# Performance work log

Hardware: AMD Instinct MI355X
Metric: run time of the kernel (lower is better)

## Reference

```python
import jax, jax.numpy as jnp
import numpy as np

B, LV, D = 8, 4096, 256   # batch, temporal length, channels
N = 2048                   # total ROIs across the batch
P = 32                     # output_size (number of output bins)
G = int(np.ceil(LV / P))   # static max adaptive sampling grid (sampling_ratio=-1)


def setup_inputs() -> dict:
    key = jax.random.key(0)
    k1, k2, k3 = jax.random.split(key, 3)
    feat = jax.random.normal(k1, (B, LV, D), dtype=jnp.float32)
    # boxes: (start, end) along the lv axis, sorted so start <= end, in [0, LV)
    boxes = jnp.sort(
        jax.random.uniform(k2, (N, 2), dtype=jnp.float32, minval=0.0, maxval=float(LV)),
        axis=1,
    )
    batch_idx = jax.random.randint(k3, (N,), 0, B, dtype=jnp.int32)
    return {"feat": feat, "boxes": boxes, "batch_idx": batch_idx}


def _roi_align_1d(feat, boxes, batch_idx):
    # Faithful 1D specialization of torchvision roi_align with boxes
    # (0, y1, 1, y2), output_size=(P, 1), aligned=True, spatial_scale=1,
    # sampling_ratio=-1. The width axis contributes a single sample at x=0
    # with weight 1, so only the y (lv) axis math remains.
    feat_flat = feat.reshape(B * LV, D)
    y1, y2 = boxes[:, 0], boxes[:, 1]
    roi_h = y2 - y1                       # aligned=True: no max(., 1) clamp
    start = y1 - 0.5                      # aligned offset
    bin_h = roi_h / P                     # [N]
    grid_h = jnp.ceil(bin_h).astype(jnp.int32)          # adaptive samples per bin
    count = jnp.maximum(grid_h, 1).astype(feat.dtype)   # avg denominator
    sub = bin_h / jnp.maximum(grid_h, 1)                # spacing inside a bin [N]
    # bin start positions: [N, P]
    bin_off = start[:, None] + jnp.arange(P, dtype=feat.dtype)[None, :] * bin_h[:, None]
    base = batch_idx.astype(jnp.int32) * LV             # [N] row offset into feat_flat

    def bilinear(y):  # y: [N, P] -> [N, P, D]
        valid = (y >= -1.0) & (y <= float(LV))
        yc = jnp.maximum(y, 0.0)
        y_lo = jnp.floor(yc).astype(jnp.int32)
        hi_case = y_lo >= LV - 1
        y_lo = jnp.where(hi_case, LV - 1, y_lo)
        y_hi = jnp.where(hi_case, LV - 1, y_lo + 1)
        yc = jnp.where(hi_case, y_lo.astype(y.dtype), yc)
        ly = yc - y_lo.astype(y.dtype)
        v = (1.0 - ly)[..., None] * feat_flat[base[:, None] + y_lo] \
            + ly[..., None] * feat_flat[base[:, None] + y_hi]
        return jnp.where(valid[..., None], v, 0.0)

    def step(acc, g):
        y = bin_off + (g.astype(feat.dtype) + 0.5) * sub[:, None]   # [N, P]
        m = (g < grid_h)[:, None, None]                              # sample active?
        return acc + jnp.where(m, bilinear(y), 0.0), None

    acc0 = jnp.zeros((N, P, D), dtype=feat.dtype)
    acc, _ = jax.lax.scan(step, acc0, jnp.arange(G, dtype=jnp.int32))
    return acc / count[:, None, None]   # [N, P, D] (torch output after transpose(1,2))


def reference(feat, boxes, batch_idx):
    return _roi_align_1d(feat, boxes, batch_idx)
```

## Files before the change

### kernel.cpp

```cpp
#include <hip/hip_runtime.h>

#define B_  8
#define LV_ 4096
#define D_  256
#define N_  2048
#define P_  32

typedef float v4f __attribute__((ext_vector_type(4)));

__device__ __forceinline__ float lane_bcast_f(float v, int l) {
    return __int_as_float(__builtin_amdgcn_readlane(__float_as_int(v), l));
}

__global__ __launch_bounds__(256) void build_order_kernel(
    const int* __restrict__ batch_idx, int* __restrict__ order)
{
    __shared__ int cnt[B_], cur[B_];
    const int tid = threadIdx.x;
    if (tid < B_) cnt[tid] = 0;
    __syncthreads();
    for (int n = tid; n < N_; n += 256) atomicAdd(&cnt[batch_idx[n]], 1);
    __syncthreads();
    if (tid == 0) {
        int s = 0;
        for (int b = 0; b < B_; ++b) { cur[b] = s; s += cnt[b]; }
    }
    __syncthreads();
    for (int n = tid; n < N_; n += 256)
        order[atomicAdd(&cur[batch_idx[n]], 1)] = n;
}

__global__ __launch_bounds__(256) void roi_rows_kernel(
    const float* __restrict__ feat,
    const float* __restrict__ boxes,
    const int*   __restrict__ batch_idx,
    const int*   __restrict__ order,
    float*       __restrict__ out)
{
    const int nwg = (N_ * P_) / 4;
    const int cpx = nwg >> 3;
    const int bid = blockIdx.x;
    const int swz = (bid & 7) * cpx + (bid >> 3);

    const int slot = (swz << 2) + (threadIdx.x >> 6);
    const int n    = order[slot >> 5];
    const int p    = slot & (P_ - 1);
    const int lane = threadIdx.x & 63;

    const float y1    = boxes[2 * n];
    const float y2    = boxes[2 * n + 1];
    const float bin_h = (y2 - y1) * (1.0f / (float)P_);
    const int   gh    = (int)ceilf(bin_h);

    const v4f* frow = (const v4f*)feat + (long)batch_idx[n] * (LV_ * (D_ / 4)) + lane;

    v4f acc = {0.f, 0.f, 0.f, 0.f};

    if (gh >= 1) {
        const float cntf    = (float)gh;
        const float sub     = bin_h / cntf;
        const float inv_sub = 1.0f / sub;
        const float halfsub = 0.5f * sub;
        const float boff    = (y1 - 0.5f) + (float)p * bin_h;
        const float a       = fmaf(0.5f, sub, boff);
        const float ylast   = fmaf(cntf - 0.5f, sub, boff);

        int r_first = (int)floorf(a);
        if (r_first < 0) r_first = 0;
        if (r_first > LV_ - 1) r_first = LV_ - 1;
        int r_last = (int)floorf(ylast) + 1;
        if (r_last > LV_ - 1) r_last = LV_ - 1;
        if (r_last < r_first) r_last = r_first;

        const float lanef = (float)lane;

        for (int base = r_first; base <= r_last; base += 64) {
            const int   r  = base + lane;
            const float d0 = ((float)base + lanef) - a;
            const float dm = d0 - 1.0f;
            const float dp = d0 + 1.0f;

            const float um = dm * inv_sub;
            const float u0 = d0 * inv_sub;
            const float up = dp * inv_sub;
            const float nm = fminf(fmaxf(ceilf(um), 0.0f), cntf);
            const float n0 = fminf(fmaxf(ceilf(u0), 0.0f), cntf);
            const float np = fminf(fmaxf(ceilf(up), 0.0f), cntf);
            float Pm = fmaf(nm, dm, -halfsub * fmaf(nm, nm, -nm));
            float P0 = fmaf(n0, d0, -halfsub * fmaf(n0, n0, -n0));
            float Pp = fmaf(np, dp, -halfsub * fmaf(np, np, -np));
            if (r == 0)       Pm = P0;
            if (r == LV_ - 1) Pp = P0 + cntf;
            const float Wl = (Pm + Pp) - 2.0f * P0;

            const int kmax = (r_last - base < 63) ? (r_last - base) : 63;
            const v4f* rp = frow + (long)base * (D_ / 4);

            int k = 0;
            for (; k + 8 <= kmax + 1; k += 8) {
                const v4f* rk = rp + (long)k * (D_ / 4);
                v4f v[8];
                #pragma unroll
                for (int j = 0; j < 8; ++j) v[j] = rk[j * (D_ / 4)];
                #pragma unroll
                for (int j = 0; j < 8; ++j) {
                    const float w = lane_bcast_f(Wl, k + j);
                    acc += v[j] * w;
                }
            }
            for (; k <= kmax; ++k) {
                const v4f v = rp[(long)k * (D_ / 4)];
                const float w = lane_bcast_f(Wl, k);
                acc += v * w;
            }
        }
    }

    const float inv_c = 1.0f / (float)(gh > 1 ? gh : 1);
    v4f res = acc * inv_c;
    v4f* op = (v4f*)out + ((long)n * P_ + p) * (D_ / 4) + lane;
    __builtin_nontemporal_store(res, op);
}

extern "C" void kernel_launch(void* const* d_in, const int* in_sizes, int n_in,
                              void* d_out, int out_size, void* d_ws, size_t ws_size,
                              hipStream_t stream) {
    const float* feat      = (const float*)d_in[0];
    const float* boxes     = (const float*)d_in[1];
    const int*   batch_idx = (const int*)d_in[2];
    float*       out       = (float*)d_out;
    int*         order     = (int*)d_ws;

    build_order_kernel<<<1, 256, 0, stream>>>(batch_idx, order);
    roi_rows_kernel<<<(N_ * P_) / 4, 256, 0, stream>>>(feat, boxes, batch_idx, order, out);
}
```

Measured before the change: 193.0 us.

## Bucket bins by 64-row window and stage shared window tile in LDS

Adds a preprocessing kernel that sorts all (roi, bin) pairs by batch and the 64-row window holding each bin's first sample row. The main kernel then handles 16 bins per 512-thread block, loads that window's feature rows into LDS once, and reads rows inside the window from LDS, falling back to global memory for rows outside it. The goal is to reuse feature rows across bins that share a window and cut global and L2 traffic. The cost is a single-block sort kernel over 65536 bins, plus load imbalance because bins have very different lengths; long bins mostly still read from global memory.

```diff
diff --git a/kernel.cpp b/kernel.cpp
--- a/kernel.cpp
+++ b/kernel.cpp
@@ -1,15 +1,56 @@
 #include <hip/hip_runtime.h>
 
-#define B_  8
-#define LV_ 4096
-#define D_  256
-#define N_  2048
-#define P_  32
+#define B_    8
+#define LV_   4096
+#define D_    256
+#define N_    2048
+#define P_    32
+#define WROWS_ 64
+#define NWIN_  (B_ * (LV_ / WROWS_))
+#define NBINS_ (N_ * P_)
+#define CPB_   16
 
 typedef float v4f __attribute__((ext_vector_type(4)));
 
 __device__ __forceinline__ float lane_bcast_f(float v, int l) {
     return __int_as_float(__builtin_amdgcn_readlane(__float_as_int(v), l));
+}
+
+__device__ __forceinline__ int bin_r_first(const float* __restrict__ boxes, int n, int p) {
+    const float y1 = boxes[2 * n], y2 = boxes[2 * n + 1];
+    const float bin_h = (y2 - y1) * (1.0f / (float)P_);
+    const int gh = (int)ceilf(bin_h);
+    if (gh < 1) return 0;
+    const float sub  = bin_h / (float)gh;
+    const float boff = (y1 - 0.5f) + (float)p * bin_h;
+    const float a    = fmaf(0.5f, sub, boff);
+    int r = (int)floorf(a);
+    if (r < 0) r = 0;
+    if (r > LV_ - 1) r = LV_ - 1;
+    return r;
+}
+
+__global__ __launch_bounds__(1024) void build_binlist_kernel(
+    const float* __restrict__ boxes, const int* __restrict__ batch_idx,
+    int* __restrict__ binlist)
+{
+    __shared__ int cnt[NWIN_], cur[NWIN_];
+    const int tid = threadIdx.x;
+    for (int i = tid; i < NWIN_; i += 1024) cnt[i] = 0;
+    __syncthreads();
+    for (int idx = tid; idx < NBINS_; idx += 1024) {
+        const int n = idx >> 5, p = idx & 31;
+        const int key = (batch_idx[n] << 6) | (bin_r_first(boxes, n, p) >> 6);
+        atomicAdd(&cnt[key], 1);
+    }
+    __syncthreads();
+    if (tid == 0) { int s = 0; for (int k = 0; k < NWIN_; ++k) { cur[k] = s; s += cnt[k]; } }
+    __syncthreads();
+    for (int idx = tid; idx < NBINS_; idx += 1024) {
+        const int n = idx >> 5, p = idx & 31;
+        const int key = (batch_idx[n] << 6) | (bin_r_first(boxes, n, p) >> 6);
+        binlist[atomicAdd(&cur[key], 1)] = idx;
+    }
 }
 
 __global__ __launch_bounds__(256) void build_order_kernel(
@@ -21,105 +62,185 @@
     __syncthreads();
     for (int n = tid; n < N_; n += 256) atomicAdd(&cnt[batch_idx[n]], 1);
     __syncthreads();
-    if (tid == 0) {
-        int s = 0;
-        for (int b = 0; b < B_; ++b) { cur[b] = s; s += cnt[b]; }
-    }
+    if (tid == 0) { int s = 0; for (int b = 0; b < B_; ++b) { cur[b] = s; s += cnt[b]; } }
     __syncthreads();
     for (int n = tid; n < N_; n += 256)
         order[atomicAdd(&cur[batch_idx[n]], 1)] = n;
 }
 
 __global__ __launch_bounds__(256) void roi_rows_kernel(
-    const float* __restrict__ feat,
-    const float* __restrict__ boxes,
-    const int*   __restrict__ batch_idx,
-    const int*   __restrict__ order,
-    float*       __restrict__ out)
+    const float* __restrict__ feat, const float* __restrict__ boxes,
+    const int* __restrict__ batch_idx, const int* __restrict__ order,
+    float* __restrict__ out)
 {
     const int nwg = (N_ * P_) / 4;
     const int cpx = nwg >> 3;
     const int bid = blockIdx.x;
     const int swz = (bid & 7) * cpx + (bid >> 3);
-
     const int slot = (swz << 2) + (threadIdx.x >> 6);
-    const int n    = order[slot >> 5];
+    const int n    = __builtin_amdgcn_readfirstlane(order[slot >> 5]);
     const int p    = slot & (P_ - 1);
     const int lane = threadIdx.x & 63;
-
-    const float y1    = boxes[2 * n];
-    const float y2    = boxes[2 * n + 1];
+    const int bi   = __builtin_amdgcn_readfirstlane(batch_idx[n]);
+    const float y1 = boxes[2 * n], y2 = boxes[2 * n + 1];
     const float bin_h = (y2 - y1) * (1.0f / (float)P_);
-    const int   gh    = (int)ceilf(bin_h);
-
-    const v4f* frow = (const v4f*)feat + (long)batch_idx[n] * (LV_ * (D_ / 4)) + lane;
-
-    v4f acc = {0.f, 0.f, 0.f, 0.f};
-
+    const int gh = (int)ceilf(bin_h);
+    const v4f* prow = (const v4f*)feat + (long)bi * (LV_ * (D_ / 4));
+    v4f acc0 = {0.f,0.f,0.f,0.f}, acc1 = {0.f,0.f,0.f,0.f};
     if (gh >= 1) {
-        const float cntf    = (float)gh;
-        const float sub     = bin_h / cntf;
-        const float inv_sub = 1.0f / sub;
+        const float cntf = (float)gh, sub = bin_h / cntf, inv_sub = 1.0f / sub;
         const float halfsub = 0.5f * sub;
-        const float boff    = (y1 - 0.5f) + (float)p * bin_h;
-        const float a       = fmaf(0.5f, sub, boff);
-        const float ylast   = fmaf(cntf - 0.5f, sub, boff);
-
+        const float boff = (y1 - 0.5f) + (float)p * bin_h;
+        const float a = fmaf(0.5f, sub, boff), ylast = fmaf(cntf - 0.5f, sub, boff);
         int r_first = (int)floorf(a);
-        if (r_first < 0) r_first = 0;
-        if (r_first > LV_ - 1) r_first = LV_ - 1;
+        if (r_first < 0) r_first = 0; if (r_first > LV_-1) r_first = LV_-1;
         int r_last = (int)floorf(ylast) + 1;
-        if (r_last > LV_ - 1) r_last = LV_ - 1;
-        if (r_last < r_first) r_last = r_first;
-
+        if (r_last > LV_-1) r_last = LV_-1; if (r_last < r_first) r_last = r_first;
+        const int r0 = __builtin_amdgcn_readfirstlane(r_first);
+        const int rl = __builtin_amdgcn_readfirstlane(r_last);
         const float lanef = (float)lane;
-
-        for (int base = r_first; base <= r_last; base += 64) {
-            const int   r  = base + lane;
+        for (int base = r0; base <= rl; base += 64) {
+            int kmax = rl - base; if (kmax > 63) kmax = 63;
+            const int r = base + lane;
             const float d0 = ((float)base + lanef) - a;
-            const float dm = d0 - 1.0f;
-            const float dp = d0 + 1.0f;
-
-            const float um = dm * inv_sub;
-            const float u0 = d0 * inv_sub;
-            const float up = dp * inv_sub;
-            const float nm = fminf(fmaxf(ceilf(um), 0.0f), cntf);
-            const float n0 = fminf(fmaxf(ceilf(u0), 0.0f), cntf);
-            const float np = fminf(fmaxf(ceilf(up), 0.0f), cntf);
+            const float dm = d0 - 1.0f, dp = d0 + 1.0f;
+            const float nm = fminf(fmaxf(ceilf(dm * inv_sub), 0.0f), cntf);
+            const float n0 = fminf(fmaxf(ceilf(d0 * inv_sub), 0.0f), cntf);
+            const float np = fminf(fmaxf(ceilf(dp * inv_sub), 0.0f), cntf);
             float Pm = fmaf(nm, dm, -halfsub * fmaf(nm, nm, -nm));
             float P0 = fmaf(n0, d0, -halfsub * fmaf(n0, n0, -n0));
             float Pp = fmaf(np, dp, -halfsub * fmaf(np, np, -np));
             if (r == 0)       Pm = P0;
             if (r == LV_ - 1) Pp = P0 + cntf;
             const float Wl = (Pm + Pp) - 2.0f * P0;
-
-            const int kmax = (r_last - base < 63) ? (r_last - base) : 63;
-            const v4f* rp = frow + (long)base * (D_ / 4);
-
+            const v4f* pS = prow + (long)base * (D_ / 4);
             int k = 0;
-            for (; k + 8 <= kmax + 1; k += 8) {
-                const v4f* rk = rp + (long)k * (D_ / 4);
-                v4f v[8];
-                #pragma unroll
-                for (int j = 0; j < 8; ++j) v[j] = rk[j * (D_ / 4)];
-                #pragma unroll
-                for (int j = 0; j < 8; ++j) {
-                    const float w = lane_bcast_f(Wl, k + j);
-                    acc += v[j] * w;
+            for (; k + 4 <= kmax + 1; k += 4) {
+                v4f v0 = pS[lane], v1 = pS[lane+64], v2 = pS[lane+128], v3 = pS[lane+192];
+                acc0 += v0 * lane_bcast_f(Wl, k);   acc1 += v1 * lane_bcast_f(Wl, k+1);
+                acc0 += v2 * lane_bcast_f(Wl, k+2); acc1 += v3 * lane_bcast_f(Wl, k+3);
+                pS += 4 * (D_ / 4);
+            }
+            for (; k <= kmax; ++k) { v4f v = pS[lane]; acc0 += v * lane_bcast_f(Wl, k); pS += (D_ / 4); }
+        }
+    }
+    const float inv_c = 1.0f / (float)(gh > 1 ? gh : 1);
+    v4f res = (acc0 + acc1) * inv_c;
+    v4f* op = (v4f*)out + ((long)n * P_ + p) * (D_ / 4) + lane;
+    __builtin_nontemporal_store(res, op);
+}
+
+__global__ __launch_bounds__(512) void roi_win_kernel(
+    const float* __restrict__ feat, const float* __restrict__ boxes,
+    const int* __restrict__ batch_idx, const int* __restrict__ binlist,
+    float* __restrict__ out)
+{
+    __shared__ v4f tile[WROWS_ * 64];
+    const int nblk = NBINS_ / CPB_;
+    const int bid  = blockIdx.x;
+    const int blk  = (bid & 7) * (nblk >> 3) + (bid >> 3);
+    const int tid  = threadIdx.x;
+    const int lane = tid & 63;
+    const int wv   = tid >> 6;
+
+    const int idx0 = binlist[blk * CPB_];
+    const int wb   = __builtin_amdgcn_readfirstlane(batch_idx[idx0 >> 5]);
+    const int wlo  = __builtin_amdgcn_readfirstlane(
+                         (bin_r_first(boxes, idx0 >> 5, idx0 & 31) >> 6) << 6);
+
+    {
+        const v4f* src = (const v4f*)feat + ((long)wb * LV_ + wlo) * (D_ / 4) + lane;
+        const int r0 = wv * 8;
+        v4f t0 = src[(r0+0)*64], t1 = src[(r0+1)*64], t2 = src[(r0+2)*64], t3 = src[(r0+3)*64];
+        v4f t4 = src[(r0+4)*64], t5 = src[(r0+5)*64], t6 = src[(r0+6)*64], t7 = src[(r0+7)*64];
+        v4f* dst = tile + r0 * 64 + lane;
+        dst[0]   = t0; dst[64]  = t1; dst[128] = t2; dst[192] = t3;
+        dst[256] = t4; dst[320] = t5; dst[384] = t6; dst[448] = t7;
+    }
+    __syncthreads();
+
+    for (int i = wv; i < CPB_; i += 8) {
+        const int idx = __builtin_amdgcn_readfirstlane(binlist[blk * CPB_ + i]);
+        const int n = idx >> 5, p = idx & 31;
+        const int bi = __builtin_amdgcn_readfirstlane(batch_idx[n]);
+
+        const float y1 = boxes[2 * n], y2 = boxes[2 * n + 1];
+        const float bin_h = (y2 - y1) * (1.0f / (float)P_);
+        const int gh = (int)ceilf(bin_h);
+
+        const v4f* prow = (const v4f*)feat + (long)bi * (LV_ * (D_ / 4));
+        v4f acc0 = {0.f,0.f,0.f,0.f}, acc1 = {0.f,0.f,0.f,0.f};
+
+        if (gh >= 1) {
+            const float cntf = (float)gh, sub = bin_h / cntf, inv_sub = 1.0f / sub;
+            const float halfsub = 0.5f * sub;
+            const float boff = (y1 - 0.5f) + (float)p * bin_h;
+            const float a = fmaf(0.5f, sub, boff), ylast = fmaf(cntf - 0.5f, sub, boff);
+
+            int r_first = (int)floorf(a);
+            if (r_first < 0) r_first = 0; if (r_first > LV_-1) r_first = LV_-1;
+            int r_last = (int)floorf(ylast) + 1;
+            if (r_last > LV_-1) r_last = LV_-1; if (r_last < r_first) r_last = r_first;
+            const int r0 = __builtin_amdgcn_readfirstlane(r_first);
+            const int rl = __builtin_amdgcn_readfirstlane(r_last);
+            const float lanef = (float)lane;
+
+            for (int gbase = r0; gbase <= rl; gbase += 64) {
+                int kmax = rl - gbase; if (kmax > 63) kmax = 63;
+
+                const int   r  = gbase + lane;
+                const float d0 = ((float)gbase + lanef) - a;
+                const float dm = d0 - 1.0f, dp = d0 + 1.0f;
+                const float nm = fminf(fmaxf(ceilf(dm * inv_sub), 0.0f), cntf);
+                const float n0 = fminf(fmaxf(ceilf(d0 * inv_sub), 0.0f), cntf);
+                const float np = fminf(fmaxf(ceilf(dp * inv_sub), 0.0f), cntf);
+                float Pm = fmaf(nm, dm, -halfsub * fmaf(nm, nm, -nm));
+                float P0 = fmaf(n0, d0, -halfsub * fmaf(n0, n0, -n0));
+                float Pp = fmaf(np, dp, -halfsub * fmaf(np, np, -np));
+                if (r == 0)       Pm = P0;
+                if (r == LV_ - 1) Pp = P0 + cntf;
+                const float Wl = (Pm + Pp) - 2.0f * P0;
+
+                const int t = kmax + 1;
+                int lo, hi;
+                if (bi == wb) {
+                    lo = wlo - gbase;          lo = lo < 0 ? 0 : (lo > t ? t : lo);
+                    hi = wlo + WROWS_ - gbase; hi = hi < lo ? lo : (hi > t ? t : hi);
+                } else { lo = t; hi = t; }
+
+#define GSEG(KS, KE) do {                                                        \
+    int k = (KS);                                                                \
+    const v4f* pS = prow + (long)(gbase + k) * (D_ / 4);                         \
+    for (; k + 4 <= (KE); k += 4) {                                              \
+        v4f v0 = pS[lane], v1 = pS[lane+64], v2 = pS[lane+128], v3 = pS[lane+192];\
+        acc0 += v0 * lane_bcast_f(Wl, k);   acc1 += v1 * lane_bcast_f(Wl, k+1);  \
+        acc0 += v2 * lane_bcast_f(Wl, k+2); acc1 += v3 * lane_bcast_f(Wl, k+3);  \
+        pS += 4 * (D_ / 4); }                                                    \
+    for (; k < (KE); ++k) { v4f v = pS[lane]; acc0 += v * lane_bcast_f(Wl, k); pS += (D_ / 4); } \
+} while (0)
+
+                GSEG(0, lo);
+                {
+                    int k = lo;
+                    const v4f* tp = tile + (gbase + lo - wlo) * 64 + lane;
+                    for (; k + 4 <= hi; k += 4) {
+                        v4f t0 = tp[0], t1 = tp[64], t2 = tp[128], t3 = tp[192];
+                        acc0 += t0 * lane_bcast_f(Wl, k);   acc1 += t1 * lane_bcast_f(Wl, k+1);
+                        acc0 += t2 * lane_bcast_f(Wl, k+2); acc1 += t3 * lane_bcast_f(Wl, k+3);
+                        tp += 256;
+                    }
+                    for (; k < hi; ++k) { acc0 += tp[0] * lane_bcast_f(Wl, k); tp += 64; }
                 }
-            }
-            for (; k <= kmax; ++k) {
-                const v4f v = rp[(long)k * (D_ / 4)];
-                const float w = lane_bcast_f(Wl, k);
-                acc += v * w;
+                GSEG(hi, t);
+#undef GSEG
             }
         }
-    }
-
-    const float inv_c = 1.0f / (float)(gh > 1 ? gh : 1);
-    v4f res = acc * inv_c;
-    v4f* op = (v4f*)out + ((long)n * P_ + p) * (D_ / 4) + lane;
-    __builtin_nontemporal_store(res, op);
+
+        const float inv_c = 1.0f / (float)(gh > 1 ? gh : 1);
+        v4f res = (acc0 + acc1) * inv_c;
+        v4f* op = (v4f*)out + ((long)n * P_ + p) * (D_ / 4) + lane;
+        __builtin_nontemporal_store(res, op);
+    }
 }
 
 extern "C" void kernel_launch(void* const* d_in, const int* in_sizes, int n_in,
@@ -129,8 +250,14 @@
     const float* boxes     = (const float*)d_in[1];
     const int*   batch_idx = (const int*)d_in[2];
     float*       out       = (float*)d_out;
-    int*         order     = (int*)d_ws;
-
-    build_order_kernel<<<1, 256, 0, stream>>>(batch_idx, order);
-    roi_rows_kernel<<<(N_ * P_) / 4, 256, 0, stream>>>(feat, boxes, batch_idx, order, out);
-}
+
+    if (ws_size >= (size_t)NBINS_ * sizeof(int)) {
+        int* binlist = (int*)d_ws;
+        build_binlist_kernel<<<1, 1024, 0, stream>>>(boxes, batch_idx, binlist);
+        roi_win_kernel<<<NBINS_ / CPB_, 512, 0, stream>>>(feat, boxes, batch_idx, binlist, out);
+    } else {
+        int* order = (int*)d_ws;
+        build_order_kernel<<<1, 256, 0, stream>>>(batch_idx, order);
+        roi_rows_kernel<<<(N_ * P_) / 4, 256, 0, stream>>>(feat, boxes, batch_idx, order, out);
+    }
+}
```

Result: slower. 233.0 us (+20.8%).
